# Performance work log

Measured on AMD Instinct MI355X. Metric: run time of the kernel, lower is better.

The kernel has to match this reference:

```python
import jax, jax.numpy as jnp
import numpy as np

IN_CH = 4
HIDDEN = 32
NNODES = 4
N_NODES_TOTAL = 4_000_000
N_EDGES = 12_000_000


def setup_inputs() -> dict:
    key = jax.random.key(0)
    ks = jax.random.split(key, 8)
    state = jax.random.normal(ks[0], (N_NODES_TOTAL, IN_CH), dtype=jnp.float32)
    edge_index = jax.random.randint(ks[1], (2, N_EDGES), 0, N_NODES_TOTAL, dtype=jnp.int64)
    s = 1.0 / np.sqrt(IN_CH)
    W_gcn = jax.random.uniform(ks[2], (IN_CH, HIDDEN), jnp.float32, -s, s)
    b_gcn = jnp.zeros((HIDDEN,), jnp.float32)
    d_in1 = IN_CH + HIDDEN
    s1 = 1.0 / np.sqrt(d_in1)
    W1 = jax.random.uniform(ks[3], (d_in1, HIDDEN), jnp.float32, -s1, s1)
    b1 = jax.random.uniform(ks[4], (HIDDEN,), jnp.float32, -s1, s1)
    s2 = 1.0 / np.sqrt(HIDDEN)
    W2 = jax.random.uniform(ks[5], (HIDDEN, 1), jnp.float32, -s2, s2)
    b2 = jax.random.uniform(ks[6], (1,), jnp.float32, -s2, s2)
    return {"state": state, "edge_index": edge_index, "W_gcn": W_gcn,
            "b_gcn": b_gcn, "W1": W1, "b1": b1, "W2": W2, "b2": b2}


def gcn_conv(x, edge_index, W, b):
    # PyG GCNConv: linear transform, add self-loops, symmetric deg normalization,
    # scatter-add messages src -> dst, then bias.
    N = x.shape[0]
    loops = jnp.arange(N, dtype=edge_index.dtype)
    src = jnp.concatenate([edge_index[0], loops])
    dst = jnp.concatenate([edge_index[1], loops])
    xw = x @ W  # [N, HIDDEN]
    deg = jnp.zeros((N,), xw.dtype).at[dst].add(jnp.ones((), xw.dtype))
    dinv = jax.lax.rsqrt(deg)  # deg >= 1 thanks to self-loops
    norm = dinv[src] * dinv[dst]  # [E+N]
    out = jnp.zeros_like(xw).at[dst].add(norm[:, None] * xw[src])
    return out + b


def reference(state, edge_index, W_gcn, b_gcn, W1, b1, W2, b2):
    x_pp = gcn_conv(state, edge_index, W_gcn, b_gcn)          # [N, HIDDEN]
    x_pp = jnp.concatenate([state, x_pp], axis=1)              # [N, IN_CH+HIDDEN]
    x_pp = x_pp.reshape(-1, NNODES, IN_CH + HIDDEN)            # [B, nnodes, F]
    v = jnp.sum(x_pp, axis=1)                                  # [B, F] sum-pool over nodes
    v = jax.nn.relu(v @ W1 + b1)
    v = v @ W2 + b2
    return v.squeeze(-1)                                       # [B]
```

## Files before the change

### kernel.cpp

```cpp
#include <hip/hip_runtime.h>

typedef unsigned long long u64;
typedef __attribute__((ext_vector_type(4))) int i32x4;
typedef __attribute__((ext_vector_type(2))) unsigned long long u64x2;

#define N_NODES   4000000
#define N_EDGES   12000000
#define N_GRAPHS  1000000

#define NBIN      977
#define GPBIN     1024
#define NPBIN     4096
#define BINCAP    14336
#define LCAP      8
#define SBLOCKS   512
#define SEPB      23440


__global__ __launch_bounds__(256) void fold_kernel(
    const float* __restrict__ Wgcn, const float* __restrict__ bgcn,
    const float* __restrict__ W1, const float* __restrict__ b1,
    float* __restrict__ fold) {
  int t = threadIdx.x;
  if (t < 128) {
    int j = t >> 2, c = t & 3;
    float s = 0.f;
    for (int k = 0; k < 32; ++k) s += Wgcn[c * 32 + k] * W1[(4 + k) * 32 + j];
    fold[j * 4 + c] = s;
  }
  if (t < 32) {
    float s = 0.f;
    for (int k = 0; k < 32; ++k) s += bgcn[k] * W1[(4 + k) * 32 + t];
    fold[128 + t] = b1[t] + 4.0f * s;
  }
}


__global__ __launch_bounds__(512) void binscatter_kernel(
    const int* __restrict__ src, const int* __restrict__ dst,
    unsigned* __restrict__ gcur, u64* __restrict__ recs) {
  extern __shared__ char smem[];
  u64* buf = (u64*)smem;
  unsigned* cnt = (unsigned*)(smem + NBIN * LCAP * 8);
  int t = threadIdx.x;
  for (int i = t; i < NBIN; i += 512) cnt[i] = 0;
  __syncthreads();
  const int base = blockIdx.x * SEPB;
  const int limit = min(SEPB, N_EDGES - base);
  const int V = limit >> 2;
  const int nrounds = (V + 511) / 512;
  const i32x4* src4 = (const i32x4*)(src + base);
  const i32x4* dst4 = (const i32x4*)(dst + base);

  i32x4 cs = {0, 0, 0, 0}, cd = {0, 0, 0, 0};
  if (t < V) { cs = __builtin_nontemporal_load(src4 + t);
               cd = __builtin_nontemporal_load(dst4 + t); }
  for (int r = 0; r < nrounds; ++r) {
    i32x4 ns = {0, 0, 0, 0}, nd = {0, 0, 0, 0};
    int nidx = (r + 1) * 512 + t;
    if (r + 1 < nrounds && nidx < V) {
      ns = __builtin_nontemporal_load(src4 + nidx);
      nd = __builtin_nontemporal_load(dst4 + nidx);
    }
    int idx = r * 512 + t;
    if (idx < V) {
#pragma unroll
      for (int k = 0; k < 4; ++k) {
        int s = cs[k];
        int d = cd[k];
        unsigned graph = (unsigned)d >> 2;
        unsigned bin   = graph >> 10;
        unsigned glo   = graph & 1023u;
        u64 rec = ((u64)glo << 32) | ((u64)((unsigned)s << 2) | (unsigned)(d & 3));
        unsigned pos = atomicAdd(&cnt[bin], 1u);
        if (pos < LCAP) buf[bin * LCAP + pos] = rec;
        else {
          unsigned p = atomicAdd(&gcur[bin], 1u);
          if (p < BINCAP) recs[(size_t)bin * BINCAP + p] = rec;
        }
      }
    }
    __syncthreads();
    bool fin = (r == nrounds - 1);
    for (int bin = t; bin < NBIN; bin += 512) {
      unsigned c = cnt[bin]; if (c > LCAP) c = LCAP;
      unsigned n = fin ? c : (c & ~3u);
      if (n) {
        unsigned pos = atomicAdd(&gcur[bin], n);
        if (pos + n <= BINCAP) {
          u64* dp = recs + (size_t)bin * BINCAP + pos;
#pragma unroll 4
          for (unsigned i = 0; i < n; ++i) dp[i] = buf[bin * LCAP + i];
        }
      }
      unsigned rem = c - n;
      for (unsigned i = 0; i < rem; ++i) buf[bin * LCAP + i] = buf[bin * LCAP + n + i];
      cnt[bin] = rem;
    }
    __syncthreads();
    cs = ns; cd = nd;
  }
}

template <bool DSI>
__global__ __launch_bounds__(512) void bindeg_kernel(
    const u64* __restrict__ recs, const unsigned* __restrict__ gcur,
    const float4* __restrict__ state4,
    float* __restrict__ dinv, float4* __restrict__ dsi4) {
  __shared__ unsigned degL[NPBIN];
  int t = threadIdx.x, bin = blockIdx.x;
  for (int i = t; i < NPBIN; i += 512) degL[i] = 0;
  __syncthreads();
  unsigned n = gcur[bin]; if (n > BINCAP) n = BINCAP;
  const u64* rp = recs + (size_t)bin * BINCAP;
  const u64x2* rv = (const u64x2*)rp;
  unsigned nv = n >> 1;
  for (unsigned i = t; i < nv; i += 512) {
    u64x2 p = __builtin_nontemporal_load(rv + i);
    unsigned lo0 = (unsigned)p.x, g0 = (unsigned)(p.x >> 32);
    unsigned lo1 = (unsigned)p.y, g1 = (unsigned)(p.y >> 32);
    atomicAdd(&degL[g0 * 4 + (lo0 & 3u)], 1u);
    atomicAdd(&degL[g1 * 4 + (lo1 & 3u)], 1u);
  }
  if ((n & 1u) && t == 0) {
    u64 v = rp[n - 1];
    atomicAdd(&degL[((unsigned)(v >> 32)) * 4 + ((unsigned)v & 3u)], 1u);
  }
  __syncthreads();
  int nb = bin * NPBIN;
  for (int i = t; i < NPBIN; i += 512) {
    int node = nb + i;
    if (node < N_NODES) {
      float dv = rsqrtf((float)(degL[i] + 1u));
      dinv[node] = dv;
      if (DSI) {
        float4 s = state4[node];
        dsi4[node] = make_float4(dv * s.x, dv * s.y, dv * s.z, dv * s.w);
      }
    }
  }
}

template <bool DSI>
__global__ __launch_bounds__(512, 4) void binreduce_kernel(
    const u64* __restrict__ recs, const unsigned* __restrict__ gcur,
    const float* __restrict__ dinv, const float4* __restrict__ dsi4,
    const float4* __restrict__ state4,
    const float* __restrict__ W1, const float* __restrict__ fold,
    const float* __restrict__ W2, const float* __restrict__ b2,
    float* __restrict__ out) {
  extern __shared__ float dynsm[];
  float* dinvL = dynsm;
  float* accL  = dynsm + NPBIN;
  __shared__ float4 w1aT[32], wg1T[32];
  __shared__ float b1p[32], w2s[32];
  int t = threadIdx.x, bin = blockIdx.x;
  if (t < 32) {
    w1aT[t] = make_float4(W1[t], W1[32 + t], W1[64 + t], W1[96 + t]);
    wg1T[t] = ((const float4*)fold)[t];
    b1p[t]  = fold[128 + t];
    w2s[t]  = W2[t];
  }
  int nb = bin * NPBIN;
  for (int i = t; i < NPBIN; i += 512) {
    int node = nb + i;
    dinvL[i] = (node < N_NODES) ? dinv[node] : 0.f;
    accL[i]  = 0.f;
  }
  __syncthreads();
  unsigned n = gcur[bin]; if (n > BINCAP) n = BINCAP;
  const u64* rp = recs + (size_t)bin * BINCAP;
  const u64x2* rv = (const u64x2*)rp;
  unsigned m = n >> 3;
  for (unsigned i = t; i < m; i += 512) {
    u64x2 p0 = __builtin_nontemporal_load(rv + i);
    u64x2 p1 = __builtin_nontemporal_load(rv + i + m);
    u64x2 p2 = __builtin_nontemporal_load(rv + i + 2 * m);
    u64x2 p3 = __builtin_nontemporal_load(rv + i + 3 * m);
    u64 r0 = p0.x, r1 = p0.y, r2 = p1.x, r3 = p1.y;
    u64 r4 = p2.x, r5 = p2.y, r6 = p3.x, r7 = p3.y;
    unsigned lo0 = (unsigned)r0, g0 = (unsigned)(r0 >> 32), s0 = lo0 >> 2;
    unsigned lo1 = (unsigned)r1, g1 = (unsigned)(r1 >> 32), s1 = lo1 >> 2;
    unsigned lo2 = (unsigned)r2, g2 = (unsigned)(r2 >> 32), s2 = lo2 >> 2;
    unsigned lo3 = (unsigned)r3, g3 = (unsigned)(r3 >> 32), s3 = lo3 >> 2;
    unsigned lo4 = (unsigned)r4, g4 = (unsigned)(r4 >> 32), s4 = lo4 >> 2;
    unsigned lo5 = (unsigned)r5, g5 = (unsigned)(r5 >> 32), s5 = lo5 >> 2;
    unsigned lo6 = (unsigned)r6, g6 = (unsigned)(r6 >> 32), s6 = lo6 >> 2;
    unsigned lo7 = (unsigned)r7, g7 = (unsigned)(r7 >> 32), s7 = lo7 >> 2;
    float4 m0, m1, m2, m3, m4, m5, m6, m7;
    float w0 = dinvL[g0 * 4 + (lo0 & 3u)];
    float w1 = dinvL[g1 * 4 + (lo1 & 3u)];
    float w2 = dinvL[g2 * 4 + (lo2 & 3u)];
    float w3 = dinvL[g3 * 4 + (lo3 & 3u)];
    float w4 = dinvL[g4 * 4 + (lo4 & 3u)];
    float w5 = dinvL[g5 * 4 + (lo5 & 3u)];
    float w6 = dinvL[g6 * 4 + (lo6 & 3u)];
    float w7 = dinvL[g7 * 4 + (lo7 & 3u)];
    if (DSI) {
      m0 = dsi4[s0]; m1 = dsi4[s1]; m2 = dsi4[s2]; m3 = dsi4[s3];
      m4 = dsi4[s4]; m5 = dsi4[s5]; m6 = dsi4[s6]; m7 = dsi4[s7];
    } else {
      m0 = state4[s0]; m1 = state4[s1]; m2 = state4[s2]; m3 = state4[s3];
      m4 = state4[s4]; m5 = state4[s5]; m6 = state4[s6]; m7 = state4[s7];
      w0 *= dinv[s0]; w1 *= dinv[s1]; w2 *= dinv[s2]; w3 *= dinv[s3];
      w4 *= dinv[s4]; w5 *= dinv[s5]; w6 *= dinv[s6]; w7 *= dinv[s7];
    }
    float* a;
    a = accL + g0 * 4;
    atomicAdd(a + 0, w0 * m0.x); atomicAdd(a + 1, w0 * m0.y);
    atomicAdd(a + 2, w0 * m0.z); atomicAdd(a + 3, w0 * m0.w);
    a = accL + g1 * 4;
    atomicAdd(a + 0, w1 * m1.x); atomicAdd(a + 1, w1 * m1.y);
    atomicAdd(a + 2, w1 * m1.z); atomicAdd(a + 3, w1 * m1.w);
    a = accL + g2 * 4;
    atomicAdd(a + 0, w2 * m2.x); atomicAdd(a + 1, w2 * m2.y);
    atomicAdd(a + 2, w2 * m2.z); atomicAdd(a + 3, w2 * m2.w);
    a = accL + g3 * 4;
    atomicAdd(a + 0, w3 * m3.x); atomicAdd(a + 1, w3 * m3.y);
    atomicAdd(a + 2, w3 * m3.z); atomicAdd(a + 3, w3 * m3.w);
    a = accL + g4 * 4;
    atomicAdd(a + 0, w4 * m4.x); atomicAdd(a + 1, w4 * m4.y);
    atomicAdd(a + 2, w4 * m4.z); atomicAdd(a + 3, w4 * m4.w);
    a = accL + g5 * 4;
    atomicAdd(a + 0, w5 * m5.x); atomicAdd(a + 1, w5 * m5.y);
    atomicAdd(a + 2, w5 * m5.z); atomicAdd(a + 3, w5 * m5.w);
    a = accL + g6 * 4;
    atomicAdd(a + 0, w6 * m6.x); atomicAdd(a + 1, w6 * m6.y);
    atomicAdd(a + 2, w6 * m6.z); atomicAdd(a + 3, w6 * m6.w);
    a = accL + g7 * 4;
    atomicAdd(a + 0, w7 * m7.x); atomicAdd(a + 1, w7 * m7.y);
    atomicAdd(a + 2, w7 * m7.z); atomicAdd(a + 3, w7 * m7.w);
  }
  unsigned done = m << 3;
  unsigned rem = n - done;
  if ((unsigned)t < rem) {
    u64 v = rp[done + t];
    unsigned lo = (unsigned)v, g = (unsigned)(v >> 32);
    unsigned s = lo >> 2;
    float w = dinvL[g * 4 + (lo & 3u)];
    float4 mm;
    if (DSI) { mm = dsi4[s]; }
    else { mm = state4[s]; w *= dinv[s]; }
    float* a = accL + g * 4;
    atomicAdd(a + 0, w * mm.x); atomicAdd(a + 1, w * mm.y);
    atomicAdd(a + 2, w * mm.z); atomicAdd(a + 3, w * mm.w);
  }
  __syncthreads();
  for (int gi = t; gi < GPBIN; gi += 512) {
    int g = bin * GPBIN + gi;
    if (g >= N_GRAPHS) break;
    float4 s0 = state4[4 * g + 0], s1 = state4[4 * g + 1];
    float4 s2 = state4[4 * g + 2], s3 = state4[4 * g + 3];
    float d0 = dinvL[gi * 4 + 0], d1 = dinvL[gi * 4 + 1];
    float d2 = dinvL[gi * 4 + 2], d3 = dinvL[gi * 4 + 3];
    float q0 = d0 * d0, q1 = d1 * d1, q2 = d2 * d2, q3 = d3 * d3;
    float ax = accL[gi * 4 + 0] + q0 * s0.x + q1 * s1.x + q2 * s2.x + q3 * s3.x;
    float ay = accL[gi * 4 + 1] + q0 * s0.y + q1 * s1.y + q2 * s2.y + q3 * s3.y;
    float az = accL[gi * 4 + 2] + q0 * s0.z + q1 * s1.z + q2 * s2.z + q3 * s3.z;
    float aw = accL[gi * 4 + 3] + q0 * s0.w + q1 * s1.w + q2 * s2.w + q3 * s3.w;
    float vx = s0.x + s1.x + s2.x + s3.x;
    float vy = s0.y + s1.y + s2.y + s3.y;
    float vz = s0.z + s1.z + s2.z + s3.z;
    float vw = s0.w + s1.w + s2.w + s3.w;
    float accum = b2[0];
#pragma unroll 4
    for (int j = 0; j < 32; ++j) {
      float4 wa = w1aT[j], wg = wg1T[j];
      float h = b1p[j]
              + vx * wa.x + vy * wa.y + vz * wa.z + vw * wa.w
              + ax * wg.x + ay * wg.y + az * wg.z + aw * wg.w;
      accum += fmaxf(h, 0.f) * w2s[j];
    }
    out[g] = accum;
  }
}


__global__ __launch_bounds__(256) void deg_kernel(
    const i32x4* __restrict__ dst4, unsigned* __restrict__ deg) {
  int stride = gridDim.x * blockDim.x;
  for (int e = blockIdx.x * blockDim.x + threadIdx.x; e < N_EDGES / 4; e += stride) {
    i32x4 d = __builtin_nontemporal_load(dst4 + e);
    atomicAdd(&deg[d.x], 1u);
    atomicAdd(&deg[d.y], 1u);
    atomicAdd(&deg[d.z], 1u);
    atomicAdd(&deg[d.w], 1u);
  }
}

__global__ __launch_bounds__(256) void dinv_kernel(unsigned* __restrict__ degdinv) {
  int i = blockIdx.x * blockDim.x + threadIdx.x;
  if (i < N_NODES) {
    float dv = rsqrtf((float)(degdinv[i] + 1u));
    reinterpret_cast<float*>(degdinv)[i] = dv;
  }
}

__global__ __launch_bounds__(256) void scatter_kernel(
    const i32x4* __restrict__ src4, const i32x4* __restrict__ dst4,
    const float* __restrict__ dinv, const float4* __restrict__ state4,
    float* __restrict__ acc) {
  int stride = gridDim.x * blockDim.x;
  for (int e = blockIdx.x * blockDim.x + threadIdx.x; e < N_EDGES / 4; e += stride) {
    i32x4 s4 = __builtin_nontemporal_load(src4 + e);
    i32x4 d4 = __builtin_nontemporal_load(dst4 + e);
#pragma unroll
    for (int u = 0; u < 4; ++u) {
      int s = (u == 0) ? s4.x : (u == 1) ? s4.y : (u == 2) ? s4.z : s4.w;
      int d = (u == 0) ? d4.x : (u == 1) ? d4.y : (u == 2) ? d4.z : d4.w;
      float w = dinv[s] * dinv[d];
      float4 st = state4[s];
      float* base = acc + (size_t)(d >> 2) * 4;
      atomicAdd(base + 0, w * st.x);
      atomicAdd(base + 1, w * st.y);
      atomicAdd(base + 2, w * st.z);
      atomicAdd(base + 3, w * st.w);
    }
  }
}

__global__ __launch_bounds__(256) void final_kernel(
    const float4* __restrict__ state4, const float4* __restrict__ dinv4,
    const float4* __restrict__ acc4, const float* __restrict__ W1,
    const float* __restrict__ fold, const float* __restrict__ W2,
    const float* __restrict__ b2, float* __restrict__ out) {
  __shared__ float4 w1aT[32];
  __shared__ float4 wg1T[32];
  __shared__ float b1p[32];
  __shared__ float w2s[32];
  int t = threadIdx.x;
  if (t < 32) {
    w1aT[t] = make_float4(W1[t], W1[32 + t], W1[64 + t], W1[96 + t]);
    wg1T[t] = ((const float4*)fold)[t];
    b1p[t]  = fold[128 + t];
    w2s[t]  = W2[t];
  }
  __syncthreads();
  int b = blockIdx.x * blockDim.x + t;
  if (b >= N_GRAPHS) return;
  float4 s0 = state4[4 * b + 0], s1 = state4[4 * b + 1];
  float4 s2 = state4[4 * b + 2], s3 = state4[4 * b + 3];
  float4 dv = dinv4[b];
  float4 a  = acc4[b];
  float q0 = dv.x * dv.x, q1 = dv.y * dv.y, q2 = dv.z * dv.z, q3 = dv.w * dv.w;
  a.x += q0 * s0.x + q1 * s1.x + q2 * s2.x + q3 * s3.x;
  a.y += q0 * s0.y + q1 * s1.y + q2 * s2.y + q3 * s3.y;
  a.z += q0 * s0.z + q1 * s1.z + q2 * s2.z + q3 * s3.z;
  a.w += q0 * s0.w + q1 * s1.w + q2 * s2.w + q3 * s3.w;
  float4 vs;
  vs.x = s0.x + s1.x + s2.x + s3.x;
  vs.y = s0.y + s1.y + s2.y + s3.y;
  vs.z = s0.z + s1.z + s2.z + s3.z;
  vs.w = s0.w + s1.w + s2.w + s3.w;
  float accum = b2[0];
#pragma unroll
  for (int j = 0; j < 32; ++j) {
    float4 wa = w1aT[j], wg = wg1T[j];
    float h = b1p[j]
            + vs.x * wa.x + vs.y * wa.y + vs.z * wa.z + vs.w * wa.w
            + a.x * wg.x + a.y * wg.y + a.z * wg.z + a.w * wg.w;
    accum += fmaxf(h, 0.f) * w2s[j];
  }
  out[b] = accum;
}


extern "C" void kernel_launch(void* const* d_in, const int* in_sizes, int n_in,
                              void* d_out, int out_size, void* d_ws, size_t ws_size,
                              hipStream_t stream) {
  const float* state = (const float*)d_in[0];
  const int*   ei    = (const int*)d_in[1];
  const float* Wgcn  = (const float*)d_in[2];
  const float* bgcn  = (const float*)d_in[3];
  const float* W1    = (const float*)d_in[4];
  const float* b1    = (const float*)d_in[5];
  const float* W2    = (const float*)d_in[6];
  const float* b2    = (const float*)d_in[7];
  float* out = (float*)d_out;

  char* ws = (char*)d_ws;
  const size_t MB = 1024u * 1024u;

  const size_t recs_bytes = (size_t)NBIN * BINCAP * 8;
  const size_t dinv_off   = recs_bytes;
  const size_t dsi_off    = dinv_off + (size_t)N_NODES * 4;
  const size_t gcur_off_d = (dsi_off + (size_t)N_NODES * 16 + 255) & ~(size_t)255;
  const size_t need_dsi   = gcur_off_d + 8192 + 1024;
  const size_t gcur_off_n = (dsi_off + 255) & ~(size_t)255;
  const size_t need_nodsi = gcur_off_n + 8192 + 1024;

  const size_t scat_smem = (size_t)NBIN * LCAP * 8 + NBIN * 4;
  const size_t red_smem  = 2 * NPBIN * 4;

  if (ws_size >= need_nodsi) {
    bool use_dsi = (ws_size >= need_dsi);
    u64*      recs = (u64*)ws;
    float*    dinv = (float*)(ws + dinv_off);
    float4*   dsi4 = (float4*)(ws + dsi_off);
    unsigned* gcur = (unsigned*)(ws + (use_dsi ? gcur_off_d : gcur_off_n));
    float*    fold = (float*)((char*)gcur + 8192);

    (void)hipMemsetAsync(gcur, 0, 8192, stream);
    fold_kernel<<<1, 128, 0, stream>>>(Wgcn, bgcn, W1, b1, fold);
    binscatter_kernel<<<SBLOCKS, 512, scat_smem, stream>>>(
        ei, ei + N_EDGES, gcur, recs);
    if (use_dsi) {
      bindeg_kernel<true><<<NBIN, 512, 0, stream>>>(
          recs, gcur, (const float4*)state, dinv, dsi4);
      binreduce_kernel<true><<<NBIN, 512, red_smem, stream>>>(
          recs, gcur, dinv, dsi4, (const float4*)state, W1, fold, W2, b2, out);
    } else {
      bindeg_kernel<false><<<NBIN, 512, 0, stream>>>(
          recs, gcur, (const float4*)state, dinv, dsi4);
      binreduce_kernel<false><<<NBIN, 512, red_smem, stream>>>(
          recs, gcur, dinv, dsi4, (const float4*)state, W1, fold, W2, b2, out);
    }
    return;
  }

  {
    unsigned* deg  = (unsigned*)ws;
    float*    acc  = (float*)(ws + 16 * MB);
    float*    fold = (float*)(ws + 32 * MB);
    (void)hipMemsetAsync(d_ws, 0, 32 * MB + 1024, stream);
    fold_kernel<<<1, 128, 0, stream>>>(Wgcn, bgcn, W1, b1, fold);
    deg_kernel<<<4096, 256, 0, stream>>>((const i32x4*)(ei + N_EDGES), deg);
    dinv_kernel<<<(N_NODES + 255) / 256, 256, 0, stream>>>(deg);
    scatter_kernel<<<8192, 256, 0, stream>>>(
        (const i32x4*)ei, (const i32x4*)(ei + N_EDGES),
        (const float*)deg, (const float4*)state, acc);
    final_kernel<<<(N_GRAPHS + 255) / 256, 256, 0, stream>>>(
        (const float4*)state, (const float4*)deg, (const float4*)acc,
        W1, fold, W2, b2, out);
  }
}
```

Baseline: 492.2 us.

## Fuse degree and reduce passes into one cooperative kernel with grid sync

Merges the per-bin degree counting and the per-bin message reduction into a single cooperative kernel, separated by a grid-wide sync after the dinv-scaled state is written. Records are read from a block's own bin twice, which may hit in cache instead of needing a second kernel launch and a reload of dinv. Also doubles per-block edge chunks and the local staging buffer in the binning scatter and narrows the reduce unroll from 8 to 4 with a higher occupancy hint. It falls back to the two-kernel path if a cooperative launch is not possible; the grid sync and the need for all 977 blocks to be co-resident add risk.

```diff
diff --git a/kernel.cpp b/kernel.cpp
--- a/kernel.cpp
+++ b/kernel.cpp
@@ -1,4 +1,7 @@
 #include <hip/hip_runtime.h>
+#include <hip/hip_cooperative_groups.h>
+
+namespace cg = cooperative_groups;
 
 typedef unsigned long long u64;
 typedef __attribute__((ext_vector_type(4))) int i32x4;
@@ -12,9 +15,9 @@
 #define GPBIN     1024
 #define NPBIN     4096
 #define BINCAP    14336
-#define LCAP      8
-#define SBLOCKS   512
-#define SEPB      23440
+#define LCAP      16
+#define SBLOCKS   256
+#define SEPB      46880
 
 
 __global__ __launch_bounds__(256) void fold_kernel(
@@ -48,35 +51,48 @@
   const int base = blockIdx.x * SEPB;
   const int limit = min(SEPB, N_EDGES - base);
   const int V = limit >> 2;
-  const int nrounds = (V + 511) / 512;
   const i32x4* src4 = (const i32x4*)(src + base);
   const i32x4* dst4 = (const i32x4*)(dst + base);
-
-  i32x4 cs = {0, 0, 0, 0}, cd = {0, 0, 0, 0};
-  if (t < V) { cs = __builtin_nontemporal_load(src4 + t);
-               cd = __builtin_nontemporal_load(dst4 + t); }
+  const int nrounds = (V + 1023) / 1024;
+
+  i32x4 cs0 = {0,0,0,0}, cd0 = {0,0,0,0}, cs1 = {0,0,0,0}, cd1 = {0,0,0,0};
+  {
+    int i0 = t, i1 = t + 512;
+    if (i0 < V) { cs0 = __builtin_nontemporal_load(src4 + i0);
+                  cd0 = __builtin_nontemporal_load(dst4 + i0); }
+    if (i1 < V) { cs1 = __builtin_nontemporal_load(src4 + i1);
+                  cd1 = __builtin_nontemporal_load(dst4 + i1); }
+  }
   for (int r = 0; r < nrounds; ++r) {
-    i32x4 ns = {0, 0, 0, 0}, nd = {0, 0, 0, 0};
-    int nidx = (r + 1) * 512 + t;
-    if (r + 1 < nrounds && nidx < V) {
-      ns = __builtin_nontemporal_load(src4 + nidx);
-      nd = __builtin_nontemporal_load(dst4 + nidx);
-    }
-    int idx = r * 512 + t;
-    if (idx < V) {
+    i32x4 ns0 = {0,0,0,0}, nd0 = {0,0,0,0}, ns1 = {0,0,0,0}, nd1 = {0,0,0,0};
+    if (r + 1 < nrounds) {
+      int j0 = (r + 1) * 1024 + t, j1 = j0 + 512;
+      if (j0 < V) { ns0 = __builtin_nontemporal_load(src4 + j0);
+                    nd0 = __builtin_nontemporal_load(dst4 + j0); }
+      if (j1 < V) { ns1 = __builtin_nontemporal_load(src4 + j1);
+                    nd1 = __builtin_nontemporal_load(dst4 + j1); }
+    }
+    int idx0 = r * 1024 + t;
 #pragma unroll
-      for (int k = 0; k < 4; ++k) {
-        int s = cs[k];
-        int d = cd[k];
-        unsigned graph = (unsigned)d >> 2;
-        unsigned bin   = graph >> 10;
-        unsigned glo   = graph & 1023u;
-        u64 rec = ((u64)glo << 32) | ((u64)((unsigned)s << 2) | (unsigned)(d & 3));
-        unsigned pos = atomicAdd(&cnt[bin], 1u);
-        if (pos < LCAP) buf[bin * LCAP + pos] = rec;
-        else {
-          unsigned p = atomicAdd(&gcur[bin], 1u);
-          if (p < BINCAP) recs[(size_t)bin * BINCAP + p] = rec;
+    for (int half = 0; half < 2; ++half) {
+      int idx = idx0 + half * 512;
+      if (idx < V) {
+        i32x4 vs = half ? cs1 : cs0;
+        i32x4 vd = half ? cd1 : cd0;
+#pragma unroll
+        for (int k = 0; k < 4; ++k) {
+          int s = vs[k];
+          int d = vd[k];
+          unsigned graph = (unsigned)d >> 2;
+          unsigned bin   = graph >> 10;
+          unsigned glo   = graph & 1023u;
+          u64 rec = ((u64)glo << 32) | ((u64)((unsigned)s << 2) | (unsigned)(d & 3));
+          unsigned pos = atomicAdd(&cnt[bin], 1u);
+          if (pos < LCAP) buf[bin * LCAP + pos] = rec;
+          else {
+            unsigned p = atomicAdd(&gcur[bin], 1u);
+            if (p < BINCAP) recs[(size_t)bin * BINCAP + p] = rec;
+          }
         }
       }
     }
@@ -84,72 +100,33 @@
     bool fin = (r == nrounds - 1);
     for (int bin = t; bin < NBIN; bin += 512) {
       unsigned c = cnt[bin]; if (c > LCAP) c = LCAP;
-      unsigned n = fin ? c : (c & ~3u);
-      if (n) {
-        unsigned pos = atomicAdd(&gcur[bin], n);
-        if (pos + n <= BINCAP) {
+      unsigned nn = fin ? c : (c & ~7u);
+      if (nn) {
+        unsigned pos = atomicAdd(&gcur[bin], nn);
+        if (pos + nn <= BINCAP) {
           u64* dp = recs + (size_t)bin * BINCAP + pos;
-#pragma unroll 4
-          for (unsigned i = 0; i < n; ++i) dp[i] = buf[bin * LCAP + i];
+          for (unsigned i2 = 0; i2 < nn; ++i2) dp[i2] = buf[bin * LCAP + i2];
         }
       }
-      unsigned rem = c - n;
-      for (unsigned i = 0; i < rem; ++i) buf[bin * LCAP + i] = buf[bin * LCAP + n + i];
-      cnt[bin] = rem;
+      unsigned rem2 = c - nn;
+      for (unsigned i2 = 0; i2 < rem2; ++i2)
+        buf[bin * LCAP + i2] = buf[bin * LCAP + nn + i2];
+      cnt[bin] = rem2;
     }
     __syncthreads();
-    cs = ns; cd = nd;
-  }
-}
-
-template <bool DSI>
-__global__ __launch_bounds__(512) void bindeg_kernel(
+    cs0 = ns0; cd0 = nd0; cs1 = ns1; cd1 = nd1;
+  }
+}
+
+
+__global__ __launch_bounds__(512, 8) void fusedreduce_kernel(
     const u64* __restrict__ recs, const unsigned* __restrict__ gcur,
-    const float4* __restrict__ state4,
-    float* __restrict__ dinv, float4* __restrict__ dsi4) {
-  __shared__ unsigned degL[NPBIN];
-  int t = threadIdx.x, bin = blockIdx.x;
-  for (int i = t; i < NPBIN; i += 512) degL[i] = 0;
-  __syncthreads();
-  unsigned n = gcur[bin]; if (n > BINCAP) n = BINCAP;
-  const u64* rp = recs + (size_t)bin * BINCAP;
-  const u64x2* rv = (const u64x2*)rp;
-  unsigned nv = n >> 1;
-  for (unsigned i = t; i < nv; i += 512) {
-    u64x2 p = __builtin_nontemporal_load(rv + i);
-    unsigned lo0 = (unsigned)p.x, g0 = (unsigned)(p.x >> 32);
-    unsigned lo1 = (unsigned)p.y, g1 = (unsigned)(p.y >> 32);
-    atomicAdd(&degL[g0 * 4 + (lo0 & 3u)], 1u);
-    atomicAdd(&degL[g1 * 4 + (lo1 & 3u)], 1u);
-  }
-  if ((n & 1u) && t == 0) {
-    u64 v = rp[n - 1];
-    atomicAdd(&degL[((unsigned)(v >> 32)) * 4 + ((unsigned)v & 3u)], 1u);
-  }
-  __syncthreads();
-  int nb = bin * NPBIN;
-  for (int i = t; i < NPBIN; i += 512) {
-    int node = nb + i;
-    if (node < N_NODES) {
-      float dv = rsqrtf((float)(degL[i] + 1u));
-      dinv[node] = dv;
-      if (DSI) {
-        float4 s = state4[node];
-        dsi4[node] = make_float4(dv * s.x, dv * s.y, dv * s.z, dv * s.w);
-      }
-    }
-  }
-}
-
-template <bool DSI>
-__global__ __launch_bounds__(512, 4) void binreduce_kernel(
-    const u64* __restrict__ recs, const unsigned* __restrict__ gcur,
-    const float* __restrict__ dinv, const float4* __restrict__ dsi4,
-    const float4* __restrict__ state4,
+    float4* __restrict__ dsi4, const float4* __restrict__ state4,
     const float* __restrict__ W1, const float* __restrict__ fold,
     const float* __restrict__ W2, const float* __restrict__ b2,
     float* __restrict__ out) {
   extern __shared__ float dynsm[];
+  unsigned* degL = (unsigned*)dynsm;
   float* dinvL = dynsm;
   float* accL  = dynsm + NPBIN;
   __shared__ float4 w1aT[32], wg1T[32];
@@ -161,50 +138,51 @@
     b1p[t]  = fold[128 + t];
     w2s[t]  = W2[t];
   }
+  for (int i = t; i < NPBIN; i += 512) { degL[i] = 0u; accL[i] = 0.f; }
+  __syncthreads();
+  unsigned n = gcur[bin]; if (n > BINCAP) n = BINCAP;
+  const u64* rp = recs + (size_t)bin * BINCAP;
+  {
+    const u64x2* rv = (const u64x2*)rp;
+    unsigned nv = n >> 1;
+    for (unsigned i = t; i < nv; i += 512) {
+      u64x2 p = __builtin_nontemporal_load(rv + i);
+      atomicAdd(&degL[((unsigned)(p.x >> 32)) * 4 + ((unsigned)p.x & 3u)], 1u);
+      atomicAdd(&degL[((unsigned)(p.y >> 32)) * 4 + ((unsigned)p.y & 3u)], 1u);
+    }
+    if ((n & 1u) && t == 0) {
+      u64 v = rp[n - 1];
+      atomicAdd(&degL[((unsigned)(v >> 32)) * 4 + ((unsigned)v & 3u)], 1u);
+    }
+  }
+  __syncthreads();
   int nb = bin * NPBIN;
   for (int i = t; i < NPBIN; i += 512) {
     int node = nb + i;
-    dinvL[i] = (node < N_NODES) ? dinv[node] : 0.f;
-    accL[i]  = 0.f;
-  }
-  __syncthreads();
-  unsigned n = gcur[bin]; if (n > BINCAP) n = BINCAP;
-  const u64* rp = recs + (size_t)bin * BINCAP;
-  const u64x2* rv = (const u64x2*)rp;
-  unsigned m = n >> 3;
-  for (unsigned i = t; i < m; i += 512) {
-    u64x2 p0 = __builtin_nontemporal_load(rv + i);
-    u64x2 p1 = __builtin_nontemporal_load(rv + i + m);
-    u64x2 p2 = __builtin_nontemporal_load(rv + i + 2 * m);
-    u64x2 p3 = __builtin_nontemporal_load(rv + i + 3 * m);
-    u64 r0 = p0.x, r1 = p0.y, r2 = p1.x, r3 = p1.y;
-    u64 r4 = p2.x, r5 = p2.y, r6 = p3.x, r7 = p3.y;
+    float dv = rsqrtf((float)(degL[i] + 1u));
+    dinvL[i] = dv;
+    if (node < N_NODES) {
+      float4 s = state4[node];
+      dsi4[node] = make_float4(dv * s.x, dv * s.y, dv * s.z, dv * s.w);
+    }
+  }
+  __threadfence();
+  cg::this_grid().sync();
+  unsigned q = n >> 2;
+  for (unsigned i = t; i < q; i += 512) {
+    u64 r0 = __builtin_nontemporal_load(rp + i);
+    u64 r1 = __builtin_nontemporal_load(rp + i + q);
+    u64 r2 = __builtin_nontemporal_load(rp + i + 2 * q);
+    u64 r3 = __builtin_nontemporal_load(rp + i + 3 * q);
     unsigned lo0 = (unsigned)r0, g0 = (unsigned)(r0 >> 32), s0 = lo0 >> 2;
     unsigned lo1 = (unsigned)r1, g1 = (unsigned)(r1 >> 32), s1 = lo1 >> 2;
     unsigned lo2 = (unsigned)r2, g2 = (unsigned)(r2 >> 32), s2 = lo2 >> 2;
     unsigned lo3 = (unsigned)r3, g3 = (unsigned)(r3 >> 32), s3 = lo3 >> 2;
-    unsigned lo4 = (unsigned)r4, g4 = (unsigned)(r4 >> 32), s4 = lo4 >> 2;
-    unsigned lo5 = (unsigned)r5, g5 = (unsigned)(r5 >> 32), s5 = lo5 >> 2;
-    unsigned lo6 = (unsigned)r6, g6 = (unsigned)(r6 >> 32), s6 = lo6 >> 2;
-    unsigned lo7 = (unsigned)r7, g7 = (unsigned)(r7 >> 32), s7 = lo7 >> 2;
-    float4 m0, m1, m2, m3, m4, m5, m6, m7;
     float w0 = dinvL[g0 * 4 + (lo0 & 3u)];
     float w1 = dinvL[g1 * 4 + (lo1 & 3u)];
     float w2 = dinvL[g2 * 4 + (lo2 & 3u)];
     float w3 = dinvL[g3 * 4 + (lo3 & 3u)];
-    float w4 = dinvL[g4 * 4 + (lo4 & 3u)];
-    float w5 = dinvL[g5 * 4 + (lo5 & 3u)];
-    float w6 = dinvL[g6 * 4 + (lo6 & 3u)];
-    float w7 = dinvL[g7 * 4 + (lo7 & 3u)];
-    if (DSI) {
-      m0 = dsi4[s0]; m1 = dsi4[s1]; m2 = dsi4[s2]; m3 = dsi4[s3];
-      m4 = dsi4[s4]; m5 = dsi4[s5]; m6 = dsi4[s6]; m7 = dsi4[s7];
-    } else {
-      m0 = state4[s0]; m1 = state4[s1]; m2 = state4[s2]; m3 = state4[s3];
-      m4 = state4[s4]; m5 = state4[s5]; m6 = state4[s6]; m7 = state4[s7];
-      w0 *= dinv[s0]; w1 *= dinv[s1]; w2 *= dinv[s2]; w3 *= dinv[s3];
-      w4 *= dinv[s4]; w5 *= dinv[s5]; w6 *= dinv[s6]; w7 *= dinv[s7];
-    }
+    float4 m0 = dsi4[s0], m1 = dsi4[s1], m2 = dsi4[s2], m3 = dsi4[s3];
     float* a;
     a = accL + g0 * 4;
     atomicAdd(a + 0, w0 * m0.x); atomicAdd(a + 1, w0 * m0.y);
@@ -218,32 +196,19 @@
     a = accL + g3 * 4;
     atomicAdd(a + 0, w3 * m3.x); atomicAdd(a + 1, w3 * m3.y);
     atomicAdd(a + 2, w3 * m3.z); atomicAdd(a + 3, w3 * m3.w);
-    a = accL + g4 * 4;
-    atomicAdd(a + 0, w4 * m4.x); atomicAdd(a + 1, w4 * m4.y);
-    atomicAdd(a + 2, w4 * m4.z); atomicAdd(a + 3, w4 * m4.w);
-    a = accL + g5 * 4;
-    atomicAdd(a + 0, w5 * m5.x); atomicAdd(a + 1, w5 * m5.y);
-    atomicAdd(a + 2, w5 * m5.z); atomicAdd(a + 3, w5 * m5.w);
-    a = accL + g6 * 4;
-    atomicAdd(a + 0, w6 * m6.x); atomicAdd(a + 1, w6 * m6.y);
-    atomicAdd(a + 2, w6 * m6.z); atomicAdd(a + 3, w6 * m6.w);
-    a = accL + g7 * 4;
-    atomicAdd(a + 0, w7 * m7.x); atomicAdd(a + 1, w7 * m7.y);
-    atomicAdd(a + 2, w7 * m7.z); atomicAdd(a + 3, w7 * m7.w);
-  }
-  unsigned done = m << 3;
-  unsigned rem = n - done;
-  if ((unsigned)t < rem) {
-    u64 v = rp[done + t];
-    unsigned lo = (unsigned)v, g = (unsigned)(v >> 32);
-    unsigned s = lo >> 2;
-    float w = dinvL[g * 4 + (lo & 3u)];
-    float4 mm;
-    if (DSI) { mm = dsi4[s]; }
-    else { mm = state4[s]; w *= dinv[s]; }
-    float* a = accL + g * 4;
-    atomicAdd(a + 0, w * mm.x); atomicAdd(a + 1, w * mm.y);
-    atomicAdd(a + 2, w * mm.z); atomicAdd(a + 3, w * mm.w);
+  }
+  {
+    unsigned done = q << 2;
+    unsigned rem = n - done;
+    if ((unsigned)t < rem) {
+      u64 v = rp[done + t];
+      unsigned lo = (unsigned)v, g = (unsigned)(v >> 32), s = lo >> 2;
+      float w = dinvL[g * 4 + (lo & 3u)];
+      float4 mm = dsi4[s];
+      float* a = accL + g * 4;
+      atomicAdd(a + 0, w * mm.x); atomicAdd(a + 1, w * mm.y);
+      atomicAdd(a + 2, w * mm.z); atomicAdd(a + 3, w * mm.w);
+    }
   }
   __syncthreads();
   for (int gi = t; gi < GPBIN; gi += 512) {
@@ -276,15 +241,146 @@
 }
 
 
+__global__ __launch_bounds__(512) void bindeg_kernel(
+    const u64* __restrict__ recs, const unsigned* __restrict__ gcur,
+    const float4* __restrict__ state4,
+    float* __restrict__ dinv, float4* __restrict__ dsi4) {
+  __shared__ unsigned degL[NPBIN];
+  int t = threadIdx.x, bin = blockIdx.x;
+  for (int i = t; i < NPBIN; i += 512) degL[i] = 0;
+  __syncthreads();
+  unsigned n = gcur[bin]; if (n > BINCAP) n = BINCAP;
+  const u64* rp = recs + (size_t)bin * BINCAP;
+  const u64x2* rv = (const u64x2*)rp;
+  unsigned nv = n >> 1;
+  for (unsigned i = t; i < nv; i += 512) {
+    u64x2 p = __builtin_nontemporal_load(rv + i);
+    atomicAdd(&degL[((unsigned)(p.x >> 32)) * 4 + ((unsigned)p.x & 3u)], 1u);
+    atomicAdd(&degL[((unsigned)(p.y >> 32)) * 4 + ((unsigned)p.y & 3u)], 1u);
+  }
+  if ((n & 1u) && t == 0) {
+    u64 v = rp[n - 1];
+    atomicAdd(&degL[((unsigned)(v >> 32)) * 4 + ((unsigned)v & 3u)], 1u);
+  }
+  __syncthreads();
+  int nb = bin * NPBIN;
+  for (int i = t; i < NPBIN; i += 512) {
+    int node = nb + i;
+    if (node < N_NODES) {
+      float dv = rsqrtf((float)(degL[i] + 1u));
+      dinv[node] = dv;
+      float4 s = state4[node];
+      dsi4[node] = make_float4(dv * s.x, dv * s.y, dv * s.z, dv * s.w);
+    }
+  }
+}
+
+__global__ __launch_bounds__(512, 8) void binreduce_kernel(
+    const u64* __restrict__ recs, const unsigned* __restrict__ gcur,
+    const float* __restrict__ dinv, const float4* __restrict__ dsi4,
+    const float4* __restrict__ state4,
+    const float* __restrict__ W1, const float* __restrict__ fold,
+    const float* __restrict__ W2, const float* __restrict__ b2,
+    float* __restrict__ out) {
+  extern __shared__ float dynsm[];
+  float* dinvL = dynsm;
+  float* accL  = dynsm + NPBIN;
+  __shared__ float4 w1aT[32], wg1T[32];
+  __shared__ float b1p[32], w2s[32];
+  int t = threadIdx.x, bin = blockIdx.x;
+  if (t < 32) {
+    w1aT[t] = make_float4(W1[t], W1[32 + t], W1[64 + t], W1[96 + t]);
+    wg1T[t] = ((const float4*)fold)[t];
+    b1p[t]  = fold[128 + t];
+    w2s[t]  = W2[t];
+  }
+  int nb = bin * NPBIN;
+  for (int i = t; i < NPBIN; i += 512) {
+    int node = nb + i;
+    dinvL[i] = (node < N_NODES) ? dinv[node] : 0.f;
+    accL[i]  = 0.f;
+  }
+  __syncthreads();
+  unsigned n = gcur[bin]; if (n > BINCAP) n = BINCAP;
+  const u64* rp = recs + (size_t)bin * BINCAP;
+  unsigned q = n >> 2;
+  for (unsigned i = t; i < q; i += 512) {
+    u64 r0 = __builtin_nontemporal_load(rp + i);
+    u64 r1 = __builtin_nontemporal_load(rp + i + q);
+    u64 r2 = __builtin_nontemporal_load(rp + i + 2 * q);
+    u64 r3 = __builtin_nontemporal_load(rp + i + 3 * q);
+    unsigned lo0 = (unsigned)r0, g0 = (unsigned)(r0 >> 32), s0 = lo0 >> 2;
+    unsigned lo1 = (unsigned)r1, g1 = (unsigned)(r1 >> 32), s1 = lo1 >> 2;
+    unsigned lo2 = (unsigned)r2, g2 = (unsigned)(r2 >> 32), s2 = lo2 >> 2;
+    unsigned lo3 = (unsigned)r3, g3 = (unsigned)(r3 >> 32), s3 = lo3 >> 2;
+    float w0 = dinvL[g0 * 4 + (lo0 & 3u)];
+    float w1 = dinvL[g1 * 4 + (lo1 & 3u)];
+    float w2 = dinvL[g2 * 4 + (lo2 & 3u)];
+    float w3 = dinvL[g3 * 4 + (lo3 & 3u)];
+    float4 m0 = dsi4[s0], m1 = dsi4[s1], m2 = dsi4[s2], m3 = dsi4[s3];
+    float* a;
+    a = accL + g0 * 4;
+    atomicAdd(a + 0, w0 * m0.x); atomicAdd(a + 1, w0 * m0.y);
+    atomicAdd(a + 2, w0 * m0.z); atomicAdd(a + 3, w0 * m0.w);
+    a = accL + g1 * 4;
+    atomicAdd(a + 0, w1 * m1.x); atomicAdd(a + 1, w1 * m1.y);
+    atomicAdd(a + 2, w1 * m1.z); atomicAdd(a + 3, w1 * m1.w);
+    a = accL + g2 * 4;
+    atomicAdd(a + 0, w2 * m2.x); atomicAdd(a + 1, w2 * m2.y);
+    atomicAdd(a + 2, w2 * m2.z); atomicAdd(a + 3, w2 * m2.w);
+    a = accL + g3 * 4;
+    atomicAdd(a + 0, w3 * m3.x); atomicAdd(a + 1, w3 * m3.y);
+    atomicAdd(a + 2, w3 * m3.z); atomicAdd(a + 3, w3 * m3.w);
+  }
+  unsigned done = q << 2;
+  unsigned rem = n - done;
+  if ((unsigned)t < rem) {
+    u64 v = rp[done + t];
+    unsigned lo = (unsigned)v, g = (unsigned)(v >> 32), s = lo >> 2;
+    float w = dinvL[g * 4 + (lo & 3u)];
+    float4 mm = dsi4[s];
+    float* a = accL + g * 4;
+    atomicAdd(a + 0, w * mm.x); atomicAdd(a + 1, w * mm.y);
+    atomicAdd(a + 2, w * mm.z); atomicAdd(a + 3, w * mm.w);
+  }
+  __syncthreads();
+  for (int gi = t; gi < GPBIN; gi += 512) {
+    int g = bin * GPBIN + gi;
+    if (g >= N_GRAPHS) break;
+    float4 s0 = state4[4 * g + 0], s1 = state4[4 * g + 1];
+    float4 s2 = state4[4 * g + 2], s3 = state4[4 * g + 3];
+    float d0 = dinvL[gi * 4 + 0], d1 = dinvL[gi * 4 + 1];
+    float d2 = dinvL[gi * 4 + 2], d3 = dinvL[gi * 4 + 3];
+    float q0 = d0 * d0, q1 = d1 * d1, q2 = d2 * d2, q3 = d3 * d3;
+    float ax = accL[gi * 4 + 0] + q0 * s0.x + q1 * s1.x + q2 * s2.x + q3 * s3.x;
+    float ay = accL[gi * 4 + 1] + q0 * s0.y + q1 * s1.y + q2 * s2.y + q3 * s3.y;
+    float az = accL[gi * 4 + 2] + q0 * s0.z + q1 * s1.z + q2 * s2.z + q3 * s3.z;
+    float aw = accL[gi * 4 + 3] + q0 * s0.w + q1 * s1.w + q2 * s2.w + q3 * s3.w;
+    float vx = s0.x + s1.x + s2.x + s3.x;
+    float vy = s0.y + s1.y + s2.y + s3.y;
+    float vz = s0.z + s1.z + s2.z + s3.z;
+    float vw = s0.w + s1.w + s2.w + s3.w;
+    float accum = b2[0];
+#pragma unroll 4
+    for (int j = 0; j < 32; ++j) {
+      float4 wa = w1aT[j], wg = wg1T[j];
+      float h = b1p[j]
+              + vx * wa.x + vy * wa.y + vz * wa.z + vw * wa.w
+              + ax * wg.x + ay * wg.y + az * wg.z + aw * wg.w;
+      accum += fmaxf(h, 0.f) * w2s[j];
+    }
+    out[g] = accum;
+  }
+}
+
+
 __global__ __launch_bounds__(256) void deg_kernel(
     const i32x4* __restrict__ dst4, unsigned* __restrict__ deg) {
   int stride = gridDim.x * blockDim.x;
   for (int e = blockIdx.x * blockDim.x + threadIdx.x; e < N_EDGES / 4; e += stride) {
     i32x4 d = __builtin_nontemporal_load(dst4 + e);
-    atomicAdd(&deg[d.x], 1u);
-    atomicAdd(&deg[d.y], 1u);
-    atomicAdd(&deg[d.z], 1u);
-    atomicAdd(&deg[d.w], 1u);
+    atomicAdd(&deg[d.x], 1u); atomicAdd(&deg[d.y], 1u);
+    atomicAdd(&deg[d.z], 1u); atomicAdd(&deg[d.w], 1u);
   }
 }
 
@@ -311,10 +407,8 @@
       float w = dinv[s] * dinv[d];
       float4 st = state4[s];
       float* base = acc + (size_t)(d >> 2) * 4;
-      atomicAdd(base + 0, w * st.x);
-      atomicAdd(base + 1, w * st.y);
-      atomicAdd(base + 2, w * st.z);
-      atomicAdd(base + 3, w * st.w);
+      atomicAdd(base + 0, w * st.x); atomicAdd(base + 1, w * st.y);
+      atomicAdd(base + 2, w * st.z); atomicAdd(base + 3, w * st.w);
     }
   }
 }
@@ -324,10 +418,8 @@
     const float4* __restrict__ acc4, const float* __restrict__ W1,
     const float* __restrict__ fold, const float* __restrict__ W2,
     const float* __restrict__ b2, float* __restrict__ out) {
-  __shared__ float4 w1aT[32];
-  __shared__ float4 wg1T[32];
-  __shared__ float b1p[32];
-  __shared__ float w2s[32];
+  __shared__ float4 w1aT[32], wg1T[32];
+  __shared__ float b1p[32], w2s[32];
   int t = threadIdx.x;
   if (t < 32) {
     w1aT[t] = make_float4(W1[t], W1[32 + t], W1[64 + t], W1[96 + t]);
@@ -384,36 +476,53 @@
   const size_t recs_bytes = (size_t)NBIN * BINCAP * 8;
   const size_t dinv_off   = recs_bytes;
   const size_t dsi_off    = dinv_off + (size_t)N_NODES * 4;
-  const size_t gcur_off_d = (dsi_off + (size_t)N_NODES * 16 + 255) & ~(size_t)255;
-  const size_t need_dsi   = gcur_off_d + 8192 + 1024;
-  const size_t gcur_off_n = (dsi_off + 255) & ~(size_t)255;
-  const size_t need_nodsi = gcur_off_n + 8192 + 1024;
+  const size_t gcur_off   = (dsi_off + (size_t)N_NODES * 16 + 255) & ~(size_t)255;
+  const size_t need_bin   = gcur_off + 8192 + 1024;
 
   const size_t scat_smem = (size_t)NBIN * LCAP * 8 + NBIN * 4;
   const size_t red_smem  = 2 * NPBIN * 4;
 
-  if (ws_size >= need_nodsi) {
-    bool use_dsi = (ws_size >= need_dsi);
-    u64*      recs = (u64*)ws;
-    float*    dinv = (float*)(ws + dinv_off);
-    float4*   dsi4 = (float4*)(ws + dsi_off);
-    unsigned* gcur = (unsigned*)(ws + (use_dsi ? gcur_off_d : gcur_off_n));
-    float*    fold = (float*)((char*)gcur + 8192);
+  if (ws_size >= need_bin) {
+    const u64*      recs = (const u64*)ws;
+    u64*            recsw = (u64*)ws;
+    float*          dinv = (float*)(ws + dinv_off);
+    float4*         dsi4 = (float4*)(ws + dsi_off);
+    unsigned*       gcur = (unsigned*)(ws + gcur_off);
+    float*          fold = (float*)(ws + gcur_off + 8192);
+    const float4*   state4 = (const float4*)state;
 
     (void)hipMemsetAsync(gcur, 0, 8192, stream);
     fold_kernel<<<1, 128, 0, stream>>>(Wgcn, bgcn, W1, b1, fold);
     binscatter_kernel<<<SBLOCKS, 512, scat_smem, stream>>>(
-        ei, ei + N_EDGES, gcur, recs);
-    if (use_dsi) {
-      bindeg_kernel<true><<<NBIN, 512, 0, stream>>>(
-          recs, gcur, (const float4*)state, dinv, dsi4);
-      binreduce_kernel<true><<<NBIN, 512, red_smem, stream>>>(
-          recs, gcur, dinv, dsi4, (const float4*)state, W1, fold, W2, b2, out);
-    } else {
-      bindeg_kernel<false><<<NBIN, 512, 0, stream>>>(
-          recs, gcur, (const float4*)state, dinv, dsi4);
-      binreduce_kernel<false><<<NBIN, 512, red_smem, stream>>>(
-          recs, gcur, dinv, dsi4, (const float4*)state, W1, fold, W2, b2, out);
+        ei, ei + N_EDGES, gcur, recsw);
+
+    bool coop_ok = false;
+    {
+      int dev = 0;
+      (void)hipGetDevice(&dev);
+      int coop_attr = 0;
+      (void)hipDeviceGetAttribute(&coop_attr, hipDeviceAttributeCooperativeLaunch, dev);
+      int numCU = 0;
+      (void)hipDeviceGetAttribute(&numCU, hipDeviceAttributeMultiprocessorCount, dev);
+      int maxblk = 0;
+      hipError_t oe = hipOccupancyMaxActiveBlocksPerMultiprocessor(
+          &maxblk, fusedreduce_kernel, 512, red_smem);
+      if (coop_attr && oe == hipSuccess && (long)maxblk * numCU >= NBIN) {
+        const float* W1p = W1; const float* foldp = fold;
+        const float* W2p = W2; const float* b2p = b2;
+        void* args[] = {(void*)&recs, (void*)&gcur, (void*)&dsi4, (void*)&state4,
+                        (void*)&W1p, (void*)&foldp, (void*)&W2p, (void*)&b2p,
+                        (void*)&out};
+        hipError_t le = hipLaunchCooperativeKernel(
+            fusedreduce_kernel, dim3(NBIN), dim3(512), args,
+            (unsigned)red_smem, stream);
+        coop_ok = (le == hipSuccess);
+      }
+    }
+    if (!coop_ok) {
+      bindeg_kernel<<<NBIN, 512, 0, stream>>>(recs, gcur, state4, dinv, dsi4);
+      binreduce_kernel<<<NBIN, 512, red_smem, stream>>>(
+          recs, gcur, dinv, dsi4, state4, W1, fold, W2, b2, out);
     }
     return;
   }
```

After: 429.7 us (median of 2 runs). 12.7% less time.
